# Kernel optimization log

Hardware: AMD Instinct MI355X
Metric: run time of the kernel (lower is better)

Reference implementation:

```python
import jax, jax.numpy as jnp
import numpy as np

L, H, D, V, T, B = 12, 12, 768, 50257, 1024, 2
HD = D // H


def _ln(x, w, b):
    m = jnp.mean(x, axis=-1, keepdims=True)
    v = jnp.var(x, axis=-1, keepdims=True)
    return (x - m) * jax.lax.rsqrt(v + 1e-5) * w + b


def setup_inputs() -> dict:
    key = jax.random.key(0)
    ks = jax.random.split(key, 8)
    def n(k, shape, std=0.02):
        return jax.random.normal(k, shape, jnp.float32) * std
    return dict(
        x=jax.random.randint(ks[0], (B, T), 0, V),
        wte=n(ks[1], (V, D), 0.01),
        wpe=n(ks[2], (T, D), 0.01),
        ln1_w=jnp.ones((L, D), jnp.float32), ln1_b=jnp.zeros((L, D), jnp.float32),
        qkv_w=n(ks[3], (L, D, 3 * D)), qkv_b=jnp.zeros((L, 3 * D), jnp.float32),
        proj_w=n(ks[4], (L, D, D)), proj_b=jnp.zeros((L, D), jnp.float32),
        ln2_w=jnp.ones((L, D), jnp.float32), ln2_b=jnp.zeros((L, D), jnp.float32),
        fc_w=n(ks[5], (L, D, 4 * D)), fc_b=jnp.zeros((L, 4 * D), jnp.float32),
        fcp_w=n(ks[6], (L, 4 * D, D)), fcp_b=jnp.zeros((L, D), jnp.float32),
        lnf_w=jnp.ones((D,), jnp.float32), lnf_b=jnp.zeros((D,), jnp.float32),
    )


def reference(x, wte, wpe, ln1_w, ln1_b, qkv_w, qkv_b, proj_w, proj_b,
              ln2_w, ln2_b, fc_w, fc_b, fcp_w, fcp_b, lnf_w, lnf_b):
    Bn, Tn = x.shape
    h = wte[x] + wpe[:Tn]                                   # [B,T,D]
    mask = jnp.tril(jnp.ones((Tn, Tn), bool))               # causal mask
    scale = 1.0 / np.sqrt(HD).astype(np.float32)

    def block(h, p):
        l1w, l1b, qw, qb, pw, pb, l2w, l2b, fw, fb, p2w, p2b = p
        a = _ln(h, l1w, l1b)
        qkv = a @ qw + qb                                    # [B,T,3D]
        q, k, v = jnp.split(qkv, 3, axis=-1)
        q = q.reshape(Bn, Tn, H, HD)
        k = k.reshape(Bn, Tn, H, HD)
        v = v.reshape(Bn, Tn, H, HD)
        att = jnp.einsum('bqhd,bkhd->bhqk', q, k) * scale    # [B,H,T,T]
        att = jnp.where(mask, att, -jnp.inf)
        att = jax.nn.softmax(att, axis=-1)
        y = jnp.einsum('bhqk,bkhd->bqhd', att, v).reshape(Bn, Tn, D)
        h = h + y @ pw + pb
        m = _ln(h, l2w, l2b)
        m = jax.nn.gelu(m @ fw + fb, approximate=True)       # tanh GELU
        h = h + m @ p2w + p2b
        return h, None

    h, _ = jax.lax.scan(block, h, (ln1_w, ln1_b, qkv_w, qkv_b, proj_w, proj_b,
                                   ln2_w, ln2_b, fc_w, fc_b, fcp_w, fcp_b))
    logits = _ln(h, lnf_w, lnf_b) @ wte.T                    # tied lm_head
    return logits
```

## Files before the change

### kernel.cpp

```cpp
#include <hip/hip_runtime.h>
#include <hip/hip_bf16.h>

typedef __hip_bfloat16 hbf16;
using bf16x8 = __attribute__((ext_vector_type(8))) __bf16;
using f32x4 = __attribute__((ext_vector_type(4))) float;

constexpr int Lc = 12, Hc = 12, Dc = 768, Vc = 50257, Tc = 1024, Bc = 2, HDc = 64;
constexpr int Mc = Bc * Tc;
constexpr int Vpad = 50304;

constexpr size_t SZ_Q = (size_t)3 * Dc * Dc;
constexpr size_t SZ_P = (size_t)Dc * Dc;
constexpr size_t SZ_F = (size_t)4 * Dc * Dc;
constexpr size_t SZ_FP = (size_t)4 * Dc * Dc;
constexpr size_t SZL = SZ_Q + SZ_P + SZ_F + SZ_FP;

#define GLD16(gp, lp)                                               \
    __builtin_amdgcn_global_load_lds(                               \
        (__attribute__((address_space(1))) void*)(void*)(gp),       \
        (__attribute__((address_space(3))) void*)(void*)(lp), 16, 0, 0)

__global__ void embed_kernel(const int* __restrict__ x, const float* __restrict__ wte,
                             const float* __restrict__ wpe, float* __restrict__ h) {
    int i = blockIdx.x * blockDim.x + threadIdx.x;
    if (i >= Mc * Dc) return;
    int m = i / Dc, d = i - m * Dc;
    int t = m % Tc;
    int tok = x[m];
    h[i] = wte[(size_t)tok * Dc + d] + wpe[(size_t)t * Dc + d];
}

__global__ __launch_bounds__(256) void ln_kernel(const float* __restrict__ x,
                                                 const float* __restrict__ w,
                                                 const float* __restrict__ b,
                                                 hbf16* __restrict__ out) {
    int wv = threadIdx.x >> 6, lane = threadIdx.x & 63;
    int row = blockIdx.x * 4 + wv;
    const float4* xr = (const float4*)(x + (size_t)row * Dc);
    float4 v[3];
    float s = 0.f, sq = 0.f;
#pragma unroll
    for (int i = 0; i < 3; i++) {
        v[i] = xr[i * 64 + lane];
        s += v[i].x + v[i].y + v[i].z + v[i].w;
        sq += v[i].x * v[i].x + v[i].y * v[i].y + v[i].z * v[i].z + v[i].w * v[i].w;
    }
#pragma unroll
    for (int o = 32; o > 0; o >>= 1) {
        s += __shfl_xor(s, o, 64);
        sq += __shfl_xor(sq, o, 64);
    }
    float mean = s * (1.f / Dc);
    float var = sq * (1.f / Dc) - mean * mean;
    float rstd = rsqrtf(var + 1e-5f);
#pragma unroll
    for (int i = 0; i < 3; i++) {
        int c = (i * 64 + lane) * 4;
        float4 wv4 = *(const float4*)(w + c);
        float4 bv4 = *(const float4*)(b + c);
        float r0 = (v[i].x - mean) * rstd * wv4.x + bv4.x;
        float r1 = (v[i].y - mean) * rstd * wv4.y + bv4.y;
        float r2 = (v[i].z - mean) * rstd * wv4.z + bv4.z;
        float r3 = (v[i].w - mean) * rstd * wv4.w + bv4.w;
        __bf16 q0 = (__bf16)r0, q1 = (__bf16)r1, q2 = (__bf16)r2, q3 = (__bf16)r3;
        ushort4 u;
        u.x = *(unsigned short*)&q0; u.y = *(unsigned short*)&q1;
        u.z = *(unsigned short*)&q2; u.w = *(unsigned short*)&q3;
        *(ushort4*)(out + (size_t)row * Dc + c) = u;
    }
}

__global__ __launch_bounds__(256) void transpose4_kernel(
    const float* __restrict__ s0, const float* __restrict__ s1,
    const float* __restrict__ s2, const float* __restrict__ s3,
    hbf16* __restrict__ d0, hbf16* __restrict__ d1,
    hbf16* __restrict__ d2, hbf16* __restrict__ d3) {
    int id = blockIdx.x;
    size_t lz = blockIdx.y;
    int bx, by, K, N;
    const float* W;
    hbf16* Wt;
    if (id < 1728)      { int t = id;        bx = t % 72; by = t / 72; K = 768;  N = 2304; W = s0 + lz * SZ_Q;  Wt = d0 + lz * SZL; }
    else if (id < 2304) { int t = id - 1728; bx = t % 24; by = t / 24; K = 768;  N = 768;  W = s1 + lz * SZ_P;  Wt = d1 + lz * SZL; }
    else if (id < 4608) { int t = id - 2304; bx = t % 96; by = t / 96; K = 768;  N = 3072; W = s2 + lz * SZ_F;  Wt = d2 + lz * SZL; }
    else                { int t = id - 4608; bx = t % 24; by = t / 24; K = 3072; N = 768;  W = s3 + lz * SZ_FP; Wt = d3 + lz * SZL; }

    __shared__ float tile[32][33];
    int n0 = bx * 32, k0 = by * 32;
    int tx = threadIdx.x & 31, ty = threadIdx.x >> 5;
#pragma unroll
    for (int i = 0; i < 4; i++) {
        int r = ty + i * 8;
        tile[r][tx] = W[(size_t)(k0 + r) * N + n0 + tx];
    }
    __syncthreads();
#pragma unroll
    for (int i = 0; i < 4; i++) {
        int r = ty + i * 8;
        Wt[(size_t)(n0 + r) * K + k0 + tx] = __float2bfloat16(tile[tx][r]);
    }
}

__global__ void convert_wte(const float* __restrict__ wte, hbf16* __restrict__ out) {
    size_t i4 = ((size_t)blockIdx.x * 256 + threadIdx.x) * 4;
    if (i4 >= (size_t)Vpad * Dc) return;
    if (i4 < (size_t)Vc * Dc) {
#pragma unroll
        for (int j = 0; j < 4; j++) out[i4 + j] = __float2bfloat16(wte[i4 + j]);
    } else {
#pragma unroll
        for (int j = 0; j < 4; j++) out[i4 + j] = __float2bfloat16(0.f);
    }
}

template <int EPI, bool OUTBF, int BN>
__global__ __launch_bounds__(256) void mm_kernel(const hbf16* __restrict__ A,
                                                 const hbf16* __restrict__ Bt,
                                                 const float* __restrict__ bias,
                                                 const float* __restrict__ resid,
                                                 void* __restrict__ Cout,
                                                 int M, int N, int K) {
    constexpr int NF = BN / 32;
    constexpr int NBI = BN / 32;
    __shared__ __bf16 As[128 * 64];
    __shared__ __bf16 Bs[BN * 64];
    int tid = threadIdx.x;
    int l = tid & 63, w = tid >> 6;
    int wr = w >> 1, wc = w & 1;

    int gx = gridDim.x, gy = gridDim.y;
    int nwg = gx * gy;
    int hwlin = blockIdx.y * gx + blockIdx.x;
    int wk = (hwlin & 7) * (nwg >> 3) + (hwlin >> 3);
    int m0 = (wk % gy) * 128;
    int n0 = (wk / gy) * BN;

    int sr = tid >> 3, sc = tid & 7;
    int scs = (sc ^ (sr & 7)) * 8;
    const hbf16* pA[4];
    __bf16* lA[4];
#pragma unroll
    for (int j = 0; j < 4; j++) {
        pA[j] = A + (size_t)(m0 + j * 32 + sr) * K + scs;
        lA[j] = As + j * 2048 + tid * 8;
    }
    const hbf16* pB[NBI];
    __bf16* lB[NBI];
#pragma unroll
    for (int j = 0; j < NBI; j++) {
        pB[j] = Bt + (size_t)(n0 + j * 32 + sr) * K + scs;
        lB[j] = Bs + j * 2048 + tid * 8;
    }

    int lr = l & 15, lg = l >> 4;
    int aoff[2][4], boff[2][NF];
#pragma unroll
    for (int kk = 0; kk < 2; kk++) {
        int ks = ((kk * 4 + lg) ^ (lr & 7)) * 8;
#pragma unroll
        for (int m = 0; m < 4; m++) aoff[kk][m] = (wr * 64 + m * 16 + lr) * 64 + ks;
#pragma unroll
        for (int n = 0; n < NF; n++) boff[kk][n] = (wc * (BN / 2) + n * 16 + lr) * 64 + ks;
    }

    f32x4 acc[4][NF] = {};

    for (int k0 = 0; k0 < K; k0 += 64) {
#pragma unroll
        for (int j = 0; j < 4; j++) {
            GLD16(pA[j], lA[j]);
            pA[j] += 64;
        }
#pragma unroll
        for (int j = 0; j < NBI; j++) {
            GLD16(pB[j], lB[j]);
            pB[j] += 64;
        }
        __syncthreads();
#pragma unroll
        for (int kk = 0; kk < 2; kk++) {
            bf16x8 af[4], bfr[NF];
#pragma unroll
            for (int m = 0; m < 4; m++) af[m] = *(const bf16x8*)&As[aoff[kk][m]];
#pragma unroll
            for (int n = 0; n < NF; n++) bfr[n] = *(const bf16x8*)&Bs[boff[kk][n]];
#pragma unroll
            for (int m = 0; m < 4; m++)
#pragma unroll
                for (int n = 0; n < NF; n++)
                    acc[m][n] = __builtin_amdgcn_mfma_f32_16x16x32_bf16(af[m], bfr[n], acc[m][n], 0, 0, 0);
        }
        __syncthreads();
    }

#pragma unroll
    for (int n = 0; n < NF; n++) {
        int col = n0 + wc * (BN / 2) + n * 16 + lr;
        bool cok = col < N;
        float bv = (bias && cok) ? bias[col] : 0.f;
#pragma unroll
        for (int m = 0; m < 4; m++) {
#pragma unroll
            for (int r = 0; r < 4; r++) {
                int row = m0 + wr * 64 + m * 16 + lg * 4 + r;
                if (!cok) continue;
                float v = acc[m][n][r] + bv;
                if (EPI == 1) v += resid[(size_t)row * N + col];
                if (EPI == 2) {
                    float x3 = v * v * v;
                    v = 0.5f * v * (1.f + tanhf(0.7978845608028654f * (v + 0.044715f * x3)));
                }
                if (OUTBF)
                    ((hbf16*)Cout)[(size_t)row * N + col] = __float2bfloat16(v);
                else
                    ((float*)Cout)[(size_t)row * N + col] = v;
            }
        }
    }
}

__global__ __launch_bounds__(512) void mm2_kernel(const hbf16* __restrict__ A,
                                                  const hbf16* __restrict__ Bt,
                                                  float* __restrict__ Cout,
                                                  int M, int N, int K) {
    __shared__ __bf16 As[256 * 64];
    __shared__ __bf16 Bs[128 * 64];
    int tid = threadIdx.x;
    int l = tid & 63, w = tid >> 6;
    int wr = w >> 1, wc = w & 1;

    int gx = gridDim.x, gy = gridDim.y;
    int nwg = gx * gy;
    int hwlin = blockIdx.y * gx + blockIdx.x;
    int wk = (hwlin & 7) * (nwg >> 3) + (hwlin >> 3);
    int m0 = (wk & 7) * 256;
    int n0 = (wk >> 3) * 128;

    int sr = tid >> 3, sc = tid & 7;
    int scs = (sc ^ (sr & 7)) * 8;
    const hbf16* pA[4];
    __bf16* lA[4];
#pragma unroll
    for (int j = 0; j < 4; j++) {
        pA[j] = A + (size_t)(m0 + j * 64 + sr) * K + scs;
        lA[j] = As + j * 4096 + tid * 8;
    }
    const hbf16* pB[2];
    __bf16* lB[2];
#pragma unroll
    for (int j = 0; j < 2; j++) {
        pB[j] = Bt + (size_t)(n0 + j * 64 + sr) * K + scs;
        lB[j] = Bs + j * 4096 + tid * 8;
    }

    int lr = l & 15, lg = l >> 4;
    int aoff[2][4], boff[2][4];
#pragma unroll
    for (int kk = 0; kk < 2; kk++) {
        int ks = ((kk * 4 + lg) ^ (lr & 7)) * 8;
#pragma unroll
        for (int m = 0; m < 4; m++) aoff[kk][m] = (wr * 64 + m * 16 + lr) * 64 + ks;
#pragma unroll
        for (int n = 0; n < 4; n++) boff[kk][n] = (wc * 64 + n * 16 + lr) * 64 + ks;
    }

    f32x4 acc[4][4] = {};

    for (int k0 = 0; k0 < K; k0 += 64) {
#pragma unroll
        for (int j = 0; j < 4; j++) {
            GLD16(pA[j], lA[j]);
            pA[j] += 64;
        }
#pragma unroll
        for (int j = 0; j < 2; j++) {
            GLD16(pB[j], lB[j]);
            pB[j] += 64;
        }
        __syncthreads();
#pragma unroll
        for (int kk = 0; kk < 2; kk++) {
            bf16x8 af[4], bfr[4];
#pragma unroll
            for (int m = 0; m < 4; m++) af[m] = *(const bf16x8*)&As[aoff[kk][m]];
#pragma unroll
            for (int n = 0; n < 4; n++) bfr[n] = *(const bf16x8*)&Bs[boff[kk][n]];
#pragma unroll
            for (int m = 0; m < 4; m++)
#pragma unroll
                for (int n = 0; n < 4; n++)
                    acc[m][n] = __builtin_amdgcn_mfma_f32_16x16x32_bf16(af[m], bfr[n], acc[m][n], 0, 0, 0);
        }
        __syncthreads();
    }

#pragma unroll
    for (int n = 0; n < 4; n++) {
        int col = n0 + wc * 64 + n * 16 + lr;
        if (col >= N) continue;
#pragma unroll
        for (int m = 0; m < 4; m++) {
#pragma unroll
            for (int r = 0; r < 4; r++) {
                int row = m0 + wr * 64 + m * 16 + lg * 4 + r;
                Cout[(size_t)row * N + col] = acc[m][n][r];
            }
        }
    }
}

__global__ __launch_bounds__(256) void fattn_kernel(const hbf16* __restrict__ qkv,
                                                    hbf16* __restrict__ y) {
    int qt = gridDim.x - 1 - blockIdx.x;
    int h = blockIdx.y, b = blockIdx.z;
    int q0 = qt * 64;
    int tid = threadIdx.x;
    int l = tid & 63, w = tid >> 6;
    int li = l & 15, lg = l >> 4;
    constexpr int RS = 3 * Dc;
    constexpr int PST = 72;
    constexpr int VST = 72;
    constexpr float SCL = 0.125f * 1.44269504f;
    constexpr float THR = 11.5f;

    __shared__ __bf16 K_lds[2][64 * 64];
    __shared__ __bf16 Vt[2][64 * VST];
    __shared__ __bf16 P_lds[4][16 * PST];

    bf16x8 qf[2];
    {
        const hbf16* qp = qkv + (size_t)(b * Tc + q0 + w * 16 + li) * RS + h * HDc + lg * 8;
        qf[0] = *(const bf16x8*)qp;
        qf[1] = *(const bf16x8*)(qp + 32);
    }

    int krow0 = tid >> 3, krow1 = 32 + (tid >> 3);
    int ks8 = tid & 7;
    int kc0 = (ks8 ^ (krow0 & 7)) * 8;
    int kc1 = (ks8 ^ (krow1 & 7)) * 8;
    const hbf16* kbase = qkv + (size_t)(b * Tc) * RS + Dc + h * HDc;

    int jp = (tid >> 3) * 2;
    int db = (tid & 7) * 8;
    const hbf16* vbase = qkv + (size_t)(b * Tc) * RS + 2 * Dc + h * HDc;

    int koff[2][4];
#pragma unroll
    for (int ks = 0; ks < 2; ks++)
#pragma unroll
        for (int n = 0; n < 4; n++)
            koff[ks][n] = (n * 16 + li) * 64 + (((ks * 4 + lg) ^ (li & 7)) * 8);

    f32x4 acc_o[4] = {};
    float m_run = -1e30f, l_run = 0.f;

    bf16x8 vr0, vr1;
    {
        const hbf16* vp = vbase + (size_t)jp * RS + db;
        vr0 = *(const bf16x8*)vp;
        vr1 = *(const bf16x8*)(vp + RS);
        GLD16(kbase + (size_t)krow0 * RS + kc0, &K_lds[0][tid * 8]);
        GLD16(kbase + (size_t)krow1 * RS + kc1, &K_lds[0][2048 + tid * 8]);
    }
#pragma unroll
    for (int i = 0; i < 8; i++) {
        __bf16 a0 = vr0[i], a1 = vr1[i];
        unsigned u = (unsigned)*(unsigned short*)&a0 | ((unsigned)*(unsigned short*)&a1 << 16);
        *(unsigned*)&Vt[0][(db + i) * VST + jp] = u;
    }

    int cur = 0;
    for (int jt = 0; jt <= qt; jt++) {
        int jn0 = (jt < qt) ? (jt + 1) * 64 : 0;

        asm volatile("s_waitcnt lgkmcnt(0)" ::: "memory");
        __builtin_amdgcn_s_barrier();

        {
            const hbf16* vp = vbase + (size_t)(jn0 + jp) * RS + db;
            vr0 = *(const bf16x8*)vp;
            vr1 = *(const bf16x8*)(vp + RS);
            GLD16(kbase + (size_t)(jn0 + krow0) * RS + kc0, &K_lds[cur ^ 1][tid * 8]);
            GLD16(kbase + (size_t)(jn0 + krow1) * RS + kc1, &K_lds[cur ^ 1][2048 + tid * 8]);
        }

        asm volatile("s_waitcnt vmcnt(4)" ::: "memory");
        __builtin_amdgcn_sched_barrier(0);

        f32x4 s[4] = {};
#pragma unroll
        for (int ks = 0; ks < 2; ks++)
#pragma unroll
            for (int n = 0; n < 4; n++) {
                bf16x8 kf = *(const bf16x8*)&K_lds[cur][koff[ks][n]];
                s[n] = __builtin_amdgcn_mfma_f32_16x16x32_bf16(kf, qf[ks], s[n], 0, 0, 0);
            }
#pragma unroll
        for (int n = 0; n < 4; n++)
#pragma unroll
            for (int r = 0; r < 4; r++) s[n][r] *= SCL;

        if (jt == qt) {
            int qloc = w * 16 + li;
#pragma unroll
            for (int n = 0; n < 4; n++)
#pragma unroll
                for (int r = 0; r < 4; r++)
                    if (n * 16 + lg * 4 + r > qloc) s[n][r] = -1e30f;
        }

        float mx = -1e30f;
#pragma unroll
        for (int n = 0; n < 4; n++)
#pragma unroll
            for (int r = 0; r < 4; r++) mx = fmaxf(mx, s[n][r]);
        mx = fmaxf(mx, __shfl_xor(mx, 16, 64));
        mx = fmaxf(mx, __shfl_xor(mx, 32, 64));

        bool dfr = __all(mx - m_run <= THR);
        float sclq = 1.f;
        if (!dfr) {
            float mnew = fmaxf(m_run, mx);
            sclq = exp2f(m_run - mnew);
            m_run = mnew;
        }
        float rs = 0.f;
#pragma unroll
        for (int n = 0; n < 4; n++)
#pragma unroll
            for (int r = 0; r < 4; r++) {
                float pv = exp2f(s[n][r] - m_run);
                s[n][r] = pv;
                rs += pv;
            }
        rs += __shfl_xor(rs, 16, 64);
        rs += __shfl_xor(rs, 32, 64);
        l_run = (dfr ? l_run : l_run * sclq) + rs;

#pragma unroll
        for (int n = 0; n < 4; n++)
#pragma unroll
            for (int r = 0; r < 4; r += 2) {
                __bf16 b0 = (__bf16)s[n][r], b1 = (__bf16)s[n][r + 1];
                unsigned u = (unsigned)*(unsigned short*)&b0 |
                             ((unsigned)*(unsigned short*)&b1 << 16);
                *(unsigned*)&P_lds[w][li * PST + n * 16 + lg * 4 + r] = u;
            }
        bf16x8 pa0 = *(const bf16x8*)&P_lds[w][li * PST + lg * 8];
        bf16x8 pa1 = *(const bf16x8*)&P_lds[w][li * PST + 32 + lg * 8];

        if (!dfr) {
#pragma unroll
            for (int r = 0; r < 4; r++) {
                float sr_ = __shfl(sclq, (l & 48) | (lg * 4 + r), 64);
#pragma unroll
                for (int n2 = 0; n2 < 4; n2++) acc_o[n2][r] *= sr_;
            }
        }

#pragma unroll
        for (int n2 = 0; n2 < 4; n2++) {
            bf16x8 vf0 = *(const bf16x8*)&Vt[cur][(n2 * 16 + li) * VST + lg * 8];
            bf16x8 vf1 = *(const bf16x8*)&Vt[cur][(n2 * 16 + li) * VST + 32 + lg * 8];
            acc_o[n2] = __builtin_amdgcn_mfma_f32_16x16x32_bf16(pa0, vf0, acc_o[n2], 0, 0, 0);
            acc_o[n2] = __builtin_amdgcn_mfma_f32_16x16x32_bf16(pa1, vf1, acc_o[n2], 0, 0, 0);
        }

#pragma unroll
        for (int i = 0; i < 8; i++) {
            __bf16 a0 = vr0[i], a1 = vr1[i];
            unsigned u = (unsigned)*(unsigned short*)&a0 | ((unsigned)*(unsigned short*)&a1 << 16);
            *(unsigned*)&Vt[cur ^ 1][(db + i) * VST + jp] = u;
        }
        cur ^= 1;
    }

#pragma unroll
    for (int r = 0; r < 4; r++) {
        float lv = __shfl(l_run, (l & 48) | (lg * 4 + r), 64);
        float rcp = 1.f / lv;
        int row = q0 + w * 16 + lg * 4 + r;
#pragma unroll
        for (int n2 = 0; n2 < 4; n2++)
            y[(size_t)(b * Tc + row) * Dc + h * HDc + n2 * 16 + li] =
                __float2bfloat16(acc_o[n2][r] * rcp);
    }
}

extern "C" void kernel_launch(void* const* d_in, const int* in_sizes, int n_in,
                              void* d_out, int out_size, void* d_ws, size_t ws_size,
                              hipStream_t stream) {
    const int* x = (const int*)d_in[0];
    const float* wte = (const float*)d_in[1];
    const float* wpe = (const float*)d_in[2];
    const float* ln1w = (const float*)d_in[3];
    const float* ln1b = (const float*)d_in[4];
    const float* qkvw = (const float*)d_in[5];
    const float* qkvb = (const float*)d_in[6];
    const float* projw = (const float*)d_in[7];
    const float* projb = (const float*)d_in[8];
    const float* ln2w = (const float*)d_in[9];
    const float* ln2b = (const float*)d_in[10];
    const float* fcw = (const float*)d_in[11];
    const float* fcb = (const float*)d_in[12];
    const float* fcpw = (const float*)d_in[13];
    const float* fcpb = (const float*)d_in[14];
    const float* lnfw = (const float*)d_in[15];
    const float* lnfb = (const float*)d_in[16];

    char* p = (char*)d_ws;
    float* h = (float*)p;     p += (size_t)Mc * Dc * 4;
    hbf16* qkv = (hbf16*)p;   p += (size_t)Mc * 3 * Dc * 2;
    hbf16* a = (hbf16*)p;     p += (size_t)Mc * Dc * 2;
    hbf16* y = (hbf16*)p;     p += (size_t)Mc * Dc * 2;
    hbf16* mlp = (hbf16*)p;   p += (size_t)Mc * 4 * Dc * 2;
    hbf16* wte_b = (hbf16*)p; p += (size_t)Vpad * Dc * 2;
    hbf16* wtr = (hbf16*)p;
    size_t used = (size_t)((char*)wtr - (char*)d_ws);
    bool all_mode = (ws_size - used) >= (size_t)Lc * SZL * 2;

    embed_kernel<<<(Mc * Dc + 255) / 256, 256, 0, stream>>>(x, wte, wpe, h);
    convert_wte<<<((size_t)Vpad * Dc / 4 + 255) / 256, 256, 0, stream>>>(wte, wte_b);

    if (all_mode) {
        transpose4_kernel<<<dim3(6912, Lc), 256, 0, stream>>>(
            qkvw, projw, fcw, fcpw,
            wtr, wtr + SZ_Q, wtr + SZ_Q + SZ_P, wtr + SZ_Q + SZ_P + SZ_F);
    }

    for (int l = 0; l < Lc; l++) {
        hbf16* base = wtr + (all_mode ? (size_t)l * SZL : 0);
        hbf16* wq_t = base;
        hbf16* wp_t = base + SZ_Q;
        hbf16* wf_t = base + SZ_Q + SZ_P;
        hbf16* wfp_t = base + SZ_Q + SZ_P + SZ_F;
        if (!all_mode) {
            transpose4_kernel<<<dim3(6912, 1), 256, 0, stream>>>(
                qkvw + (size_t)l * SZ_Q, projw + (size_t)l * SZ_P,
                fcw + (size_t)l * SZ_F, fcpw + (size_t)l * SZ_FP,
                wq_t, wp_t, wf_t, wfp_t);
        }

        ln_kernel<<<Mc / 4, 256, 0, stream>>>(h, ln1w + (size_t)l * Dc, ln1b + (size_t)l * Dc, a);
        mm_kernel<0, true, 128><<<dim3(3 * Dc / 128, Mc / 128), 256, 0, stream>>>(
            a, wq_t, qkvb + (size_t)l * 3 * Dc, nullptr, qkv, Mc, 3 * Dc, Dc);
        fattn_kernel<<<dim3(Tc / 64, Hc, Bc), 256, 0, stream>>>(qkv, y);
        mm_kernel<1, false, 64><<<dim3(Dc / 64, Mc / 128), 256, 0, stream>>>(
            y, wp_t, projb + (size_t)l * Dc, h, h, Mc, Dc, Dc);
        ln_kernel<<<Mc / 4, 256, 0, stream>>>(h, ln2w + (size_t)l * Dc, ln2b + (size_t)l * Dc, a);
        mm_kernel<2, true, 128><<<dim3(4 * Dc / 128, Mc / 128), 256, 0, stream>>>(
            a, wf_t, fcb + (size_t)l * 4 * Dc, nullptr, mlp, Mc, 4 * Dc, Dc);
        mm_kernel<1, false, 64><<<dim3(Dc / 64, Mc / 128), 256, 0, stream>>>(
            mlp, wfp_t, fcpb + (size_t)l * Dc, h, h, Mc, Dc, 4 * Dc);
    }

    ln_kernel<<<Mc / 4, 256, 0, stream>>>(h, lnfw, lnfb, a);
    mm2_kernel<<<dim3(Vpad / 128, Mc / 256), 512, 0, stream>>>(
        a, wte_b, (float*)d_out, Mc, Vc, Dc);
}
```

Before: 2.371 ms.

## Double-buffer LDS tiles in GEMM kernels to overlap global loads with MFMA

Both GEMM kernels (mm_kernel and mm2_kernel) now keep two LDS buffers for A and B. The next K-tile is prefetched with global_load_lds while the current tile feeds the MFMAs, using explicit vmcnt waits and raw s_barrier calls. This is meant to hide global memory latency that the previous load, sync, compute, sync loop exposed. It doubles LDS use per block, which may lower occupancy. It also depends on hand-tuned vmcnt counts and on the barrier being safe without a full __syncthreads fence.

```diff
diff --git a/kernel.cpp b/kernel.cpp
--- a/kernel.cpp
+++ b/kernel.cpp
@@ -122,8 +122,8 @@
                                                  int M, int N, int K) {
     constexpr int NF = BN / 32;
     constexpr int NBI = BN / 32;
-    __shared__ __bf16 As[128 * 64];
-    __shared__ __bf16 Bs[BN * 64];
+    __shared__ __bf16 As[2][128 * 64];
+    __shared__ __bf16 Bs[2][BN * 64];
     int tid = threadIdx.x;
     int l = tid & 63, w = tid >> 6;
     int wr = w >> 1, wc = w & 1;
@@ -138,19 +138,18 @@
     int sr = tid >> 3, sc = tid & 7;
     int scs = (sc ^ (sr & 7)) * 8;
     const hbf16* pA[4];
-    __bf16* lA[4];
-#pragma unroll
-    for (int j = 0; j < 4; j++) {
-        pA[j] = A + (size_t)(m0 + j * 32 + sr) * K + scs;
-        lA[j] = As + j * 2048 + tid * 8;
-    }
+#pragma unroll
+    for (int j = 0; j < 4; j++) pA[j] = A + (size_t)(m0 + j * 32 + sr) * K + scs;
     const hbf16* pB[NBI];
-    __bf16* lB[NBI];
-#pragma unroll
-    for (int j = 0; j < NBI; j++) {
-        pB[j] = Bt + (size_t)(n0 + j * 32 + sr) * K + scs;
-        lB[j] = Bs + j * 2048 + tid * 8;
-    }
+#pragma unroll
+    for (int j = 0; j < NBI; j++) pB[j] = Bt + (size_t)(n0 + j * 32 + sr) * K + scs;
+
+    auto stage = [&](int bi, int ko) {
+#pragma unroll
+        for (int j = 0; j < 4; j++) GLD16(pA[j] + ko, &As[bi][j * 2048 + tid * 8]);
+#pragma unroll
+        for (int j = 0; j < NBI; j++) GLD16(pB[j] + ko, &Bs[bi][j * 2048 + tid * 8]);
+    };
 
     int lr = l & 15, lg = l >> 4;
     int aoff[2][4], boff[2][NF];
@@ -164,33 +163,37 @@
     }
 
     f32x4 acc[4][NF] = {};
-
-    for (int k0 = 0; k0 < K; k0 += 64) {
-#pragma unroll
-        for (int j = 0; j < 4; j++) {
-            GLD16(pA[j], lA[j]);
-            pA[j] += 64;
-        }
-#pragma unroll
-        for (int j = 0; j < NBI; j++) {
-            GLD16(pB[j], lB[j]);
-            pB[j] += 64;
-        }
-        __syncthreads();
+    int nk = K / 64;
+
+    stage(0, 0);
+    for (int t = 0; t < nk; ++t) {
+        int cur = t & 1;
+        if (t + 1 < nk) {
+            stage(cur ^ 1, (t + 1) * 64);
+            if constexpr (BN == 128)
+                asm volatile("s_waitcnt vmcnt(8)" ::: "memory");
+            else
+                asm volatile("s_waitcnt vmcnt(6)" ::: "memory");
+        } else {
+            asm volatile("s_waitcnt vmcnt(0)" ::: "memory");
+        }
+        __builtin_amdgcn_sched_barrier(0);
+        __builtin_amdgcn_s_barrier();
+        __builtin_amdgcn_sched_barrier(0);
 #pragma unroll
         for (int kk = 0; kk < 2; kk++) {
             bf16x8 af[4], bfr[NF];
 #pragma unroll
-            for (int m = 0; m < 4; m++) af[m] = *(const bf16x8*)&As[aoff[kk][m]];
-#pragma unroll
-            for (int n = 0; n < NF; n++) bfr[n] = *(const bf16x8*)&Bs[boff[kk][n]];
+            for (int m = 0; m < 4; m++) af[m] = *(const bf16x8*)&As[cur][aoff[kk][m]];
+#pragma unroll
+            for (int n = 0; n < NF; n++) bfr[n] = *(const bf16x8*)&Bs[cur][boff[kk][n]];
 #pragma unroll
             for (int m = 0; m < 4; m++)
 #pragma unroll
                 for (int n = 0; n < NF; n++)
                     acc[m][n] = __builtin_amdgcn_mfma_f32_16x16x32_bf16(af[m], bfr[n], acc[m][n], 0, 0, 0);
         }
-        __syncthreads();
+        __builtin_amdgcn_s_barrier();
     }
 
 #pragma unroll
@@ -223,8 +226,8 @@
                                                   const hbf16* __restrict__ Bt,
                                                   float* __restrict__ Cout,
                                                   int M, int N, int K) {
-    __shared__ __bf16 As[256 * 64];
-    __shared__ __bf16 Bs[128 * 64];
+    __shared__ __bf16 As[2][256 * 64];
+    __shared__ __bf16 Bs[2][128 * 64];
     int tid = threadIdx.x;
     int l = tid & 63, w = tid >> 6;
     int wr = w >> 1, wc = w & 1;
@@ -239,19 +242,18 @@
     int sr = tid >> 3, sc = tid & 7;
     int scs = (sc ^ (sr & 7)) * 8;
     const hbf16* pA[4];
-    __bf16* lA[4];
-#pragma unroll
-    for (int j = 0; j < 4; j++) {
-        pA[j] = A + (size_t)(m0 + j * 64 + sr) * K + scs;
-        lA[j] = As + j * 4096 + tid * 8;
-    }
+#pragma unroll
+    for (int j = 0; j < 4; j++) pA[j] = A + (size_t)(m0 + j * 64 + sr) * K + scs;
     const hbf16* pB[2];
-    __bf16* lB[2];
-#pragma unroll
-    for (int j = 0; j < 2; j++) {
-        pB[j] = Bt + (size_t)(n0 + j * 64 + sr) * K + scs;
-        lB[j] = Bs + j * 4096 + tid * 8;
-    }
+#pragma unroll
+    for (int j = 0; j < 2; j++) pB[j] = Bt + (size_t)(n0 + j * 64 + sr) * K + scs;
+
+    auto stage = [&](int bi, int ko) {
+#pragma unroll
+        for (int j = 0; j < 4; j++) GLD16(pA[j] + ko, &As[bi][j * 4096 + tid * 8]);
+#pragma unroll
+        for (int j = 0; j < 2; j++) GLD16(pB[j] + ko, &Bs[bi][j * 4096 + tid * 8]);
+    };
 
     int lr = l & 15, lg = l >> 4;
     int aoff[2][4], boff[2][4];
@@ -265,33 +267,34 @@
     }
 
     f32x4 acc[4][4] = {};
-
-    for (int k0 = 0; k0 < K; k0 += 64) {
-#pragma unroll
-        for (int j = 0; j < 4; j++) {
-            GLD16(pA[j], lA[j]);
-            pA[j] += 64;
-        }
-#pragma unroll
-        for (int j = 0; j < 2; j++) {
-            GLD16(pB[j], lB[j]);
-            pB[j] += 64;
-        }
-        __syncthreads();
+    int nk = K / 64;
+
+    stage(0, 0);
+    for (int t = 0; t < nk; ++t) {
+        int cur = t & 1;
+        if (t + 1 < nk) {
+            stage(cur ^ 1, (t + 1) * 64);
+            asm volatile("s_waitcnt vmcnt(6)" ::: "memory");
+        } else {
+            asm volatile("s_waitcnt vmcnt(0)" ::: "memory");
+        }
+        __builtin_amdgcn_sched_barrier(0);
+        __builtin_amdgcn_s_barrier();
+        __builtin_amdgcn_sched_barrier(0);
 #pragma unroll
         for (int kk = 0; kk < 2; kk++) {
             bf16x8 af[4], bfr[4];
 #pragma unroll
-            for (int m = 0; m < 4; m++) af[m] = *(const bf16x8*)&As[aoff[kk][m]];
-#pragma unroll
-            for (int n = 0; n < 4; n++) bfr[n] = *(const bf16x8*)&Bs[boff[kk][n]];
+            for (int m = 0; m < 4; m++) af[m] = *(const bf16x8*)&As[cur][aoff[kk][m]];
+#pragma unroll
+            for (int n = 0; n < 4; n++) bfr[n] = *(const bf16x8*)&Bs[cur][boff[kk][n]];
 #pragma unroll
             for (int m = 0; m < 4; m++)
 #pragma unroll
                 for (int n = 0; n < 4; n++)
                     acc[m][n] = __builtin_amdgcn_mfma_f32_16x16x32_bf16(af[m], bfr[n], acc[m][n], 0, 0, 0);
         }
-        __syncthreads();
+        __builtin_amdgcn_s_barrier();
     }
 
 #pragma unroll
```

Result: no change. 2.344 ms (-1.1%).
